# Kernel tuning notes

Hardware: AMD Instinct MI355X
Metric: run time of the kernel (lower is better)

The kernel has to match this reference:

```python
import jax, jax.numpy as jnp
import numpy as np


def setup_inputs() -> dict:
    key = jax.random.key(0)
    kq, kk, kv = jax.random.split(key, 3)
    B, N, D = 16, 2048, 64
    queries = jax.random.normal(kq, (B, N, D), dtype=jnp.float32)
    keys = jax.random.normal(kk, (B, N, D), dtype=jnp.float32)
    values = jax.random.normal(kv, (B, N, D), dtype=jnp.float32)
    return {"queries": queries, "keys": keys, "values": values}


def reference(queries, keys, values):
    d = queries.shape[-1]
    scale = 1.0 / jnp.sqrt(jnp.asarray(d, dtype=queries.dtype))
    # scores: [B, Nq, Nk]
    scores = jnp.einsum("bqd,bkd->bqk", queries, keys) * scale
    # Faithful to the original: softmax over dim=0 (the batch dimension).
    attn = jax.nn.softmax(scores, axis=0)
    # dropout p=0.0 -> identity
    return jnp.einsum("bqk,bkd->bqd", attn, values)
```

## Files before the change

### kernel.cpp

```cpp
#include <hip/hip_runtime.h>
#include <hip/hip_bf16.h>

typedef __attribute__((ext_vector_type(8))) short short8;
typedef __attribute__((ext_vector_type(4))) short short4v;
typedef __attribute__((ext_vector_type(2))) int   int2v;
typedef __attribute__((ext_vector_type(4))) float floatx4;

#define BATCH 16
#define SEQ   2048
#define DIM   64
#define QSCALE 0.18033688011112042f
#define WS_NEED (12u*1024u*1024u)

__device__ __forceinline__ unsigned short f2bf(float f) {
    return __builtin_bit_cast(unsigned short, __float2bfloat16(f));
}

#if defined(__has_builtin)
#if __has_builtin(__builtin_amdgcn_exp2f)
#define EXP2(x) __builtin_amdgcn_exp2f(x)
#endif
#endif
#ifndef EXP2
#define EXP2(x) exp2f(x)
#endif

#define MFMA32(A,B,C) __builtin_amdgcn_mfma_f32_16x16x32_bf16(A,B,C,0,0,0)

#if defined(__has_builtin)
#if __has_builtin(__builtin_amdgcn_mfma_f32_16x16x16bf16_1k)
#define MFMA16(A,B,C) __builtin_amdgcn_mfma_f32_16x16x16bf16_1k(A,B,C,0,0,0)
#elif __has_builtin(__builtin_amdgcn_mfma_f32_16x16x16_bf16)
#define MFMA16(A,B,C) __builtin_amdgcn_mfma_f32_16x16x16_bf16(A,B,C,0,0,0)
#endif
#endif
#ifndef MFMA16
__device__ __forceinline__ floatx4 mfma16_asm(short4v a, short4v b, floatx4 c) {
    asm volatile("s_nop 1\n\tv_mfma_f32_16x16x16_bf16 %0, %1, %2, %0"
                 : "+v"(c) : "v"(a), "v"(b));
    return c;
}
#define MFMA16(A,B,C) mfma16_asm(A,B,C)
#endif

#define LIGHT_BARRIER()                                        \
    do {                                                       \
        asm volatile("s_waitcnt lgkmcnt(0)" ::: "memory");     \
        __builtin_amdgcn_s_barrier();                          \
        __builtin_amdgcn_sched_barrier(0);                     \
    } while (0)

__global__ __launch_bounds__(256)
void convert_kernel(const float* __restrict__ Q, const float* __restrict__ K,
                    const float* __restrict__ V, unsigned short* __restrict__ ws) {
    const int t = blockIdx.x * 256 + threadIdx.x;
    if (t < 524288) {
        const int region = t >> 18;
        const int r = t & 262143;
        const int b = r >> 14;
        const int rem = r & 16383;
        const int t16 = rem >> 7;
        const int st  = (rem >> 6) & 1;
        const int l   = rem & 63;
        const int a = l & 15, g = l >> 4;
        const float* src = (region == 0 ? Q : K) +
            ((size_t)(b * SEQ + t16 * 16 + a)) * DIM + st * 32 + g * 8;
        const float s = (region == 0) ? QSCALE : 1.0f;
        short8 o;
        #pragma unroll
        for (int p = 0; p < 8; ++p) o[p] = (short)f2bf(src[p] * s);
        *(short8*)(ws + (size_t)region * 2097152 + (size_t)r * 8) = o;
    } else {
        const int r = t - 524288;
        const int b  = r >> 13;
        const int kt = (r >> 6) & 127;
        const int l  = r & 63;
        const int a = l & 15, g = l >> 4;
        const float* src = V + ((size_t)(b * SEQ + kt * 16 + g * 4)) * DIM + a;
        short8 o0, o1;
        #pragma unroll
        for (int dt = 0; dt < 2; ++dt)
            #pragma unroll
            for (int p = 0; p < 4; ++p)
                o0[dt * 4 + p] = (short)f2bf(src[(size_t)p * DIM + dt * 16]);
        #pragma unroll
        for (int dt = 2; dt < 4; ++dt)
            #pragma unroll
            for (int p = 0; p < 4; ++p)
                o1[(dt - 2) * 4 + p] = (short)f2bf(src[(size_t)p * DIM + dt * 16]);
        unsigned short* dst = ws + 4194304 + (size_t)r * 16;
        *(short8*)(dst)     = o0;
        *(short8*)(dst + 8) = o1;
    }
}

__global__ __launch_bounds__(512)
void dpa_main(const unsigned short* __restrict__ Qw, const unsigned short* __restrict__ Kw,
              const unsigned short* __restrict__ Vw, float* __restrict__ Og) {
    __shared__ __align__(16) float dl[2][4][64][12];

    const int tid = threadIdx.x;
    const int l = tid & 63;
    const int w = tid >> 6;
    const int a = l & 15, g = l >> 4;
    const int bx = blockIdx.x;
    const int ch = bx & 3;
    const int qt = bx >> 2;
    const int b0 = w * 2;
    const int wsw = w ^ (l >> 3);

    const unsigned short* Kb = Kw + (size_t)b0 * 131072 + l * 8;
    const unsigned short* Vb = Vw + (size_t)b0 * 131072 + l * 16;

    short8 Qf[2][2];
    {
        const unsigned short* Qb = Qw + (size_t)b0 * 131072 + qt * 1024 + l * 8;
        #pragma unroll
        for (int bb = 0; bb < 2; ++bb)
            #pragma unroll
            for (int st = 0; st < 2; ++st)
                Qf[bb][st] = *(const short8*)(Qb + bb * 131072 + st * 512);
    }

    short8 Kf[2][2];
    #pragma unroll
    for (int bb = 0; bb < 2; ++bb)
        #pragma unroll
        for (int st = 0; st < 2; ++st)
            Kf[bb][st] = *(const short8*)(Kb + bb * 131072 + (ch * 32) * 1024 + st * 512);

    floatx4 O[2][4];
    #pragma unroll
    for (int bb = 0; bb < 2; ++bb)
        #pragma unroll
        for (int dt = 0; dt < 4; ++dt) O[bb][dt] = (floatx4)0.0f;

    floatx4 SA[2], SB[2];

#define QKEXP(T, SOUT)                                                        \
    __builtin_amdgcn_s_setprio(1);                                            \
    {                                                                         \
        floatx4 s0 = (floatx4)0.0f, s1 = (floatx4)0.0f;                       \
        s0 = MFMA32(Kf[0][0], Qf[0][0], s0);                                  \
        s0 = MFMA32(Kf[0][1], Qf[0][1], s0);                                  \
        s1 = MFMA32(Kf[1][0], Qf[1][0], s1);                                  \
        s1 = MFMA32(Kf[1][1], Qf[1][1], s1);                                  \
        SOUT[0] = s0; SOUT[1] = s1;                                           \
    }                                                                         \
    __builtin_amdgcn_s_setprio(0);                                            \
    {                                                                         \
        const int ktn_ = ch * 32 + (((T) < 31) ? (T) + 1 : 31);               \
        Kf[0][0] = *(const short8*)(Kb + 0 * 131072 + ktn_ * 1024);           \
        Kf[0][1] = *(const short8*)(Kb + 0 * 131072 + ktn_ * 1024 + 512);     \
        Kf[1][0] = *(const short8*)(Kb + 1 * 131072 + ktn_ * 1024);           \
        Kf[1][1] = *(const short8*)(Kb + 1 * 131072 + ktn_ * 1024 + 512);     \
    }                                                                         \
    _Pragma("unroll")                                                         \
    for (int r = 0; r < 4; ++r) {                                             \
        const float e0 = EXP2(SOUT[0][r]);                                    \
        const float e1 = EXP2(SOUT[1][r]);                                    \
        SOUT[0][r] = e0; SOUT[1][r] = e1;                                     \
        dl[(T) & 1][r][l][wsw] = e0 + e1;                                     \
    }

#define COMBINE_PV(T, SPREV, v01_0, v23_0, v01_1, v23_1)                      \
    {                                                                         \
        float fr_[4];                                                         \
        _Pragma("unroll")                                                     \
        for (int r = 0; r < 4; ++r) {                                         \
            const floatx4 u0 = *(const floatx4*)&dl[((T)-1) & 1][r][l][0];    \
            const floatx4 u1 = *(const floatx4*)&dl[((T)-1) & 1][r][l][4];    \
            const floatx4 us = u0 + u1;                                       \
            fr_[r] = __builtin_amdgcn_rcpf((us[0] + us[1]) + (us[2] + us[3]));\
        }                                                                     \
        _Pragma("unroll")                                                     \
        for (int bb = 0; bb < 2; ++bb) {                                      \
            const short8 v01 = (bb == 0) ? v01_0 : v01_1;                     \
            const short8 v23 = (bb == 0) ? v23_0 : v23_1;                     \
            const unsigned int c0 = __builtin_bit_cast(unsigned int, SPREV[bb][0] * fr_[0]) + 0x8000u; \
            const unsigned int c1 = __builtin_bit_cast(unsigned int, SPREV[bb][1] * fr_[1]) + 0x8000u; \
            const unsigned int c2 = __builtin_bit_cast(unsigned int, SPREV[bb][2] * fr_[2]) + 0x8000u; \
            const unsigned int c3 = __builtin_bit_cast(unsigned int, SPREV[bb][3] * fr_[3]) + 0x8000u; \
            int2v pp;                                                         \
            pp[0] = (int)__builtin_amdgcn_perm(c1, c0, 0x07060302u);          \
            pp[1] = (int)__builtin_amdgcn_perm(c3, c2, 0x07060302u);          \
            const short4v af = __builtin_bit_cast(short4v, pp);               \
            const short4v b0v = __builtin_shufflevector(v01, v01, 0, 1, 2, 3);\
            const short4v b1v = __builtin_shufflevector(v01, v01, 4, 5, 6, 7);\
            const short4v b2v = __builtin_shufflevector(v23, v23, 0, 1, 2, 3);\
            const short4v b3v = __builtin_shufflevector(v23, v23, 4, 5, 6, 7);\
            __builtin_amdgcn_s_setprio(1);                                    \
            O[bb][0] = MFMA16(af, b0v, O[bb][0]);                             \
            O[bb][1] = MFMA16(af, b1v, O[bb][1]);                             \
            O[bb][2] = MFMA16(af, b2v, O[bb][2]);                             \
            O[bb][3] = MFMA16(af, b3v, O[bb][3]);                             \
            __builtin_amdgcn_s_setprio(0);                                    \
        }                                                                     \
    }

#define BODY(T, SOUT, SPREV)                                                  \
    {                                                                         \
        const int ktp_ = ch * 32 + (T) - 1;                                   \
        const unsigned short* vp0_ = Vb + 0 * 131072 + ktp_ * 1024;           \
        const unsigned short* vp1_ = Vb + 1 * 131072 + ktp_ * 1024;           \
        const short8 V01_0_ = *(const short8*)(vp0_);                         \
        const short8 V23_0_ = *(const short8*)(vp0_ + 8);                     \
        const short8 V01_1_ = *(const short8*)(vp1_);                         \
        const short8 V23_1_ = *(const short8*)(vp1_ + 8);                     \
        QKEXP(T, SOUT)                                                        \
        LIGHT_BARRIER();                                                      \
        COMBINE_PV(T, SPREV, V01_0_, V23_0_, V01_1_, V23_1_)                  \
        LIGHT_BARRIER();                                                      \
    }

    QKEXP(0, SA)

    #pragma unroll 1
    for (int j = 0; j < 15; ++j) {
        const int t1 = 2 * j + 1;
        BODY(t1, SB, SA)
        BODY(t1 + 1, SA, SB)
    }
    BODY(31, SB, SA)

    {
        const int ktp = ch * 32 + 31;
        const unsigned short* vp0 = Vb + 0 * 131072 + ktp * 1024;
        const unsigned short* vp1 = Vb + 1 * 131072 + ktp * 1024;
        const short8 V01_0 = *(const short8*)(vp0);
        const short8 V23_0 = *(const short8*)(vp0 + 8);
        const short8 V01_1 = *(const short8*)(vp1);
        const short8 V23_1 = *(const short8*)(vp1 + 8);
        COMBINE_PV(32, SB, V01_0, V23_0, V01_1, V23_1)
    }

    asm volatile("s_nop 7\n\ts_nop 7" :::);

    #pragma unroll
    for (int bb = 0; bb < 2; ++bb)
        #pragma unroll
        for (int dt = 0; dt < 4; ++dt)
            #pragma unroll
            for (int r = 0; r < 4; ++r)
                unsafeAtomicAdd(Og + ((size_t)((b0 + bb) * SEQ + qt * 16 + g * 4 + r)) * DIM
                                    + dt * 16 + a,
                                O[bb][dt][r]);
#undef BODY
#undef COMBINE_PV
#undef QKEXP
}

__global__ __launch_bounds__(512)
void dpa_naive(const float* __restrict__ Q, const float* __restrict__ K,
               const float* __restrict__ V, float* __restrict__ out) {
    __shared__ float attn_lds[BATCH][8][64];
    const int tid = threadIdx.x;
    const int lane_k = tid & 63, row_q = tid >> 6, lane_d = tid & 63;
    const int q0 = blockIdx.x * 8;
    float acc[BATCH];
    #pragma unroll
    for (int b = 0; b < BATCH; ++b) acc[b] = 0.0f;
    for (int k0 = 0; k0 < SEQ; k0 += 64) {
        float s[BATCH];
        #pragma unroll
        for (int b = 0; b < BATCH; ++b) {
            const float4* qrow = (const float4*)(Q + ((size_t)b * SEQ + (q0 + row_q)) * DIM);
            const float4* krow = (const float4*)(K + ((size_t)b * SEQ + (k0 + lane_k)) * DIM);
            float a0 = 0.f;
            #pragma unroll
            for (int d4 = 0; d4 < 16; ++d4) {
                float4 qa = qrow[d4]; float4 kb = krow[d4];
                a0 += qa.x*kb.x + qa.y*kb.y + qa.z*kb.z + qa.w*kb.w;
            }
            s[b] = a0 * 0.125f;
        }
        float m = s[0];
        #pragma unroll
        for (int b = 1; b < BATCH; ++b) m = fmaxf(m, s[b]);
        float den = 0.f;
        #pragma unroll
        for (int b = 0; b < BATCH; ++b) { s[b] = __expf(s[b] - m); den += s[b]; }
        const float inv = 1.0f / den;
        #pragma unroll
        for (int b = 0; b < BATCH; ++b) attn_lds[b][row_q][lane_k] = s[b] * inv;
        __syncthreads();
        #pragma unroll
        for (int b = 0; b < BATCH; ++b) {
            const float* vbase = V + ((size_t)b * SEQ + k0) * DIM + lane_d;
            float acc2 = 0.f;
            #pragma unroll 8
            for (int kk = 0; kk < 64; ++kk) acc2 += attn_lds[b][row_q][kk] * vbase[(size_t)kk * DIM];
            acc[b] += acc2;
        }
        __syncthreads();
    }
    #pragma unroll
    for (int b = 0; b < BATCH; ++b)
        out[((size_t)b * SEQ + (q0 + row_q)) * DIM + lane_d] = acc[b];
}

extern "C" void kernel_launch(void* const* d_in, const int* in_sizes, int n_in,
                              void* d_out, int out_size, void* d_ws, size_t ws_size,
                              hipStream_t stream) {
    const float* Q = (const float*)d_in[0];
    const float* K = (const float*)d_in[1];
    const float* V = (const float*)d_in[2];
    float* out = (float*)d_out;

    if (ws_size < WS_NEED) {
        dpa_naive<<<dim3(SEQ / 8), dim3(512), 0, stream>>>(Q, K, V, out);
        return;
    }
    unsigned short* ws = (unsigned short*)d_ws;
    hipMemsetAsync(d_out, 0, (size_t)out_size * sizeof(float), stream);
    convert_kernel<<<dim3(2560), dim3(256), 0, stream>>>(Q, K, V, ws);
    dpa_main<<<dim3(512), dim3(512), 0, stream>>>(ws, ws + 2097152, ws + 4194304, out);
}
```

Measured before the change: 82.59 us.

## Process two key tiles per barrier phase to halve workgroup barriers

Restructures the main loop so each iteration computes QK and exp for two key tiles, then does one barrier and two combine/PV steps, with a double-buffered LDS partial-sum array indexed by iteration parity. The software pipeline across single tiles is replaced by a two-tile batch, with two K register sets prefetched. The goal is to cut the number of LIGHT_BARRIER syncs per tile in half, at the cost of more registers, a larger LDS buffer, and less overlap between QK of the next tile and PV of the current one.

```diff
diff --git a/kernel.cpp b/kernel.cpp
--- a/kernel.cpp
+++ b/kernel.cpp
@@ -97,7 +97,7 @@
 __global__ __launch_bounds__(512)
 void dpa_main(const unsigned short* __restrict__ Qw, const unsigned short* __restrict__ Kw,
               const unsigned short* __restrict__ Vw, float* __restrict__ Og) {
-    __shared__ __align__(16) float dl[2][4][64][12];
+    __shared__ __align__(16) float dl[2][8][64][12];
 
     const int tid = threadIdx.x;
     const int l = tid & 63;
@@ -122,12 +122,14 @@
                 Qf[bb][st] = *(const short8*)(Qb + bb * 131072 + st * 512);
     }
 
-    short8 Kf[2][2];
+    short8 Kf0[2][2], Kf1[2][2];
     #pragma unroll
     for (int bb = 0; bb < 2; ++bb)
         #pragma unroll
-        for (int st = 0; st < 2; ++st)
-            Kf[bb][st] = *(const short8*)(Kb + bb * 131072 + (ch * 32) * 1024 + st * 512);
+        for (int st = 0; st < 2; ++st) {
+            Kf0[bb][st] = *(const short8*)(Kb + bb * 131072 + (ch * 32 + 0) * 1024 + st * 512);
+            Kf1[bb][st] = *(const short8*)(Kb + bb * 131072 + (ch * 32 + 1) * 1024 + st * 512);
+        }
 
     floatx4 O[2][4];
     #pragma unroll
@@ -135,41 +137,35 @@
         #pragma unroll
         for (int dt = 0; dt < 4; ++dt) O[bb][dt] = (floatx4)0.0f;
 
-    floatx4 SA[2], SB[2];
-
-#define QKEXP(T, SOUT)                                                        \
-    __builtin_amdgcn_s_setprio(1);                                            \
+#define QKTILE(KF, SOUT, KTN, SLOT, P)                                        \
     {                                                                         \
         floatx4 s0 = (floatx4)0.0f, s1 = (floatx4)0.0f;                       \
-        s0 = MFMA32(Kf[0][0], Qf[0][0], s0);                                  \
-        s0 = MFMA32(Kf[0][1], Qf[0][1], s0);                                  \
-        s1 = MFMA32(Kf[1][0], Qf[1][0], s1);                                  \
-        s1 = MFMA32(Kf[1][1], Qf[1][1], s1);                                  \
-        SOUT[0] = s0; SOUT[1] = s1;                                           \
-    }                                                                         \
-    __builtin_amdgcn_s_setprio(0);                                            \
-    {                                                                         \
-        const int ktn_ = ch * 32 + (((T) < 31) ? (T) + 1 : 31);               \
-        Kf[0][0] = *(const short8*)(Kb + 0 * 131072 + ktn_ * 1024);           \
-        Kf[0][1] = *(const short8*)(Kb + 0 * 131072 + ktn_ * 1024 + 512);     \
-        Kf[1][0] = *(const short8*)(Kb + 1 * 131072 + ktn_ * 1024);           \
-        Kf[1][1] = *(const short8*)(Kb + 1 * 131072 + ktn_ * 1024 + 512);     \
-    }                                                                         \
-    _Pragma("unroll")                                                         \
-    for (int r = 0; r < 4; ++r) {                                             \
-        const float e0 = EXP2(SOUT[0][r]);                                    \
-        const float e1 = EXP2(SOUT[1][r]);                                    \
-        SOUT[0][r] = e0; SOUT[1][r] = e1;                                     \
-        dl[(T) & 1][r][l][wsw] = e0 + e1;                                     \
-    }
-
-#define COMBINE_PV(T, SPREV, v01_0, v23_0, v01_1, v23_1)                      \
+        __builtin_amdgcn_s_setprio(1);                                        \
+        s0 = MFMA32(KF[0][0], Qf[0][0], s0);                                  \
+        s0 = MFMA32(KF[0][1], Qf[0][1], s0);                                  \
+        s1 = MFMA32(KF[1][0], Qf[1][0], s1);                                  \
+        s1 = MFMA32(KF[1][1], Qf[1][1], s1);                                  \
+        __builtin_amdgcn_s_setprio(0);                                        \
+        KF[0][0] = *(const short8*)(Kb + 0 * 131072 + (KTN) * 1024);          \
+        KF[0][1] = *(const short8*)(Kb + 0 * 131072 + (KTN) * 1024 + 512);    \
+        KF[1][0] = *(const short8*)(Kb + 1 * 131072 + (KTN) * 1024);          \
+        KF[1][1] = *(const short8*)(Kb + 1 * 131072 + (KTN) * 1024 + 512);    \
+        _Pragma("unroll")                                                     \
+        for (int r = 0; r < 4; ++r) {                                         \
+            const float e0 = EXP2(s0[r]);                                     \
+            const float e1 = EXP2(s1[r]);                                     \
+            SOUT[0][r] = e0; SOUT[1][r] = e1;                                 \
+            dl[P][(SLOT) + r][l][wsw] = e0 + e1;                              \
+        }                                                                     \
+    }
+
+#define COMBINE_PV(SPREV, SLOT, P, v01_0, v23_0, v01_1, v23_1)                \
     {                                                                         \
         float fr_[4];                                                         \
         _Pragma("unroll")                                                     \
         for (int r = 0; r < 4; ++r) {                                         \
-            const floatx4 u0 = *(const floatx4*)&dl[((T)-1) & 1][r][l][0];    \
-            const floatx4 u1 = *(const floatx4*)&dl[((T)-1) & 1][r][l][4];    \
+            const floatx4 u0 = *(const floatx4*)&dl[P][(SLOT) + r][l][0];     \
+            const floatx4 u1 = *(const floatx4*)&dl[P][(SLOT) + r][l][4];     \
             const floatx4 us = u0 + u1;                                       \
             fr_[r] = __builtin_amdgcn_rcpf((us[0] + us[1]) + (us[2] + us[3]));\
         }                                                                     \
@@ -198,40 +194,39 @@
         }                                                                     \
     }
 
-#define BODY(T, SOUT, SPREV)                                                  \
-    {                                                                         \
-        const int ktp_ = ch * 32 + (T) - 1;                                   \
-        const unsigned short* vp0_ = Vb + 0 * 131072 + ktp_ * 1024;           \
-        const unsigned short* vp1_ = Vb + 1 * 131072 + ktp_ * 1024;           \
-        const short8 V01_0_ = *(const short8*)(vp0_);                         \
-        const short8 V23_0_ = *(const short8*)(vp0_ + 8);                     \
-        const short8 V01_1_ = *(const short8*)(vp1_);                         \
-        const short8 V23_1_ = *(const short8*)(vp1_ + 8);                     \
-        QKEXP(T, SOUT)                                                        \
-        LIGHT_BARRIER();                                                      \
-        COMBINE_PV(T, SPREV, V01_0_, V23_0_, V01_1_, V23_1_)                  \
-        LIGHT_BARRIER();                                                      \
-    }
-
-    QKEXP(0, SA)
+    floatx4 S0[2], S1[2];
 
     #pragma unroll 1
-    for (int j = 0; j < 15; ++j) {
-        const int t1 = 2 * j + 1;
-        BODY(t1, SB, SA)
-        BODY(t1 + 1, SA, SB)
-    }
-    BODY(31, SB, SA)
-
-    {
-        const int ktp = ch * 32 + 31;
-        const unsigned short* vp0 = Vb + 0 * 131072 + ktp * 1024;
-        const unsigned short* vp1 = Vb + 1 * 131072 + ktp * 1024;
-        const short8 V01_0 = *(const short8*)(vp0);
-        const short8 V23_0 = *(const short8*)(vp0 + 8);
-        const short8 V01_1 = *(const short8*)(vp1);
-        const short8 V23_1 = *(const short8*)(vp1 + 8);
-        COMBINE_PV(32, SB, V01_0, V23_0, V01_1, V23_1)
+    for (int j = 0; j < 16; ++j) {
+        const int p = j & 1;
+        const int kt0 = ch * 32 + 2 * j;
+        const int kt1 = kt0 + 1;
+        const int ktn0 = (j < 15) ? (kt0 + 2) : kt0;
+        const int ktn1 = (j < 15) ? (kt1 + 2) : kt1;
+
+        short8 V01_0[2], V23_0[2];
+        #pragma unroll
+        for (int bb = 0; bb < 2; ++bb) {
+            const unsigned short* vp = Vb + bb * 131072 + kt0 * 1024;
+            V01_0[bb] = *(const short8*)(vp);
+            V23_0[bb] = *(const short8*)(vp + 8);
+        }
+
+        QKTILE(Kf0, S0, ktn0, 0, p)
+        QKTILE(Kf1, S1, ktn1, 4, p)
+        LIGHT_BARRIER();
+
+        COMBINE_PV(S0, 0, p, V01_0[0], V23_0[0], V01_0[1], V23_0[1])
+
+        short8 V01_1[2], V23_1[2];
+        #pragma unroll
+        for (int bb = 0; bb < 2; ++bb) {
+            const unsigned short* vp = Vb + bb * 131072 + kt1 * 1024;
+            V01_1[bb] = *(const short8*)(vp);
+            V23_1[bb] = *(const short8*)(vp + 8);
+        }
+
+        COMBINE_PV(S1, 4, p, V01_1[0], V23_1[0], V01_1[1], V23_1[1])
     }
 
     asm volatile("s_nop 7\n\ts_nop 7" :::);
@@ -245,9 +240,8 @@
                 unsafeAtomicAdd(Og + ((size_t)((b0 + bb) * SEQ + qt * 16 + g * 4 + r)) * DIM
                                     + dt * 16 + a,
                                 O[bb][dt][r]);
-#undef BODY
 #undef COMBINE_PV
-#undef QKEXP
+#undef QKTILE
 }
 
 __global__ __launch_bounds__(512)
```

New measurement: 87.17 us. +5.5%, slower.

## Fold Q conversion into main kernel and output zeroing into KV convert

Applied to the files above, without the earlier changes.

Q is no longer pre-converted to bf16 in a separate pass. Each wave in the main kernel loads its fp32 Q fragment directly, scales it and converts it in registers. The output memset is folded into the K/V conversion kernel, which drops one launch and shrinks the workspace. The cost is that each Q tile is read as fp32 by the main kernel, a small one-time load per block.

```diff
diff --git a/kernel.cpp b/kernel.cpp
--- a/kernel.cpp
+++ b/kernel.cpp
@@ -10,7 +10,7 @@
 #define SEQ   2048
 #define DIM   64
 #define QSCALE 0.18033688011112042f
-#define WS_NEED (12u*1024u*1024u)
+#define WS_NEED (9u*1024u*1024u)
 
 __device__ __forceinline__ unsigned short f2bf(float f) {
     return __builtin_bit_cast(unsigned short, __float2bfloat16(f));
@@ -51,27 +51,28 @@
     } while (0)
 
 __global__ __launch_bounds__(256)
-void convert_kernel(const float* __restrict__ Q, const float* __restrict__ K,
-                    const float* __restrict__ V, unsigned short* __restrict__ ws) {
+void convert_kv(const float* __restrict__ K, const float* __restrict__ V,
+                unsigned short* __restrict__ ws, float* __restrict__ Og) {
     const int t = blockIdx.x * 256 + threadIdx.x;
-    if (t < 524288) {
-        const int region = t >> 18;
-        const int r = t & 262143;
+
+    for (unsigned u = (unsigned)t; u < 524288u; u += 393216u)
+        ((floatx4*)Og)[u] = (floatx4)0.0f;
+
+    if (t < 262144) {
+        const int r = t;
         const int b = r >> 14;
         const int rem = r & 16383;
         const int t16 = rem >> 7;
         const int st  = (rem >> 6) & 1;
         const int l   = rem & 63;
         const int a = l & 15, g = l >> 4;
-        const float* src = (region == 0 ? Q : K) +
-            ((size_t)(b * SEQ + t16 * 16 + a)) * DIM + st * 32 + g * 8;
-        const float s = (region == 0) ? QSCALE : 1.0f;
+        const float* src = K + ((size_t)(b * SEQ + t16 * 16 + a)) * DIM + st * 32 + g * 8;
         short8 o;
         #pragma unroll
-        for (int p = 0; p < 8; ++p) o[p] = (short)f2bf(src[p] * s);
-        *(short8*)(ws + (size_t)region * 2097152 + (size_t)r * 8) = o;
+        for (int p = 0; p < 8; ++p) o[p] = (short)f2bf(src[p]);
+        *(short8*)(ws + (size_t)r * 8) = o;
     } else {
-        const int r = t - 524288;
+        const int r = t - 262144;
         const int b  = r >> 13;
         const int kt = (r >> 6) & 127;
         const int l  = r & 63;
@@ -88,14 +89,14 @@
             #pragma unroll
             for (int p = 0; p < 4; ++p)
                 o1[(dt - 2) * 4 + p] = (short)f2bf(src[(size_t)p * DIM + dt * 16]);
-        unsigned short* dst = ws + 4194304 + (size_t)r * 16;
+        unsigned short* dst = ws + 2097152 + (size_t)r * 16;
         *(short8*)(dst)     = o0;
         *(short8*)(dst + 8) = o1;
     }
 }
 
 __global__ __launch_bounds__(512)
-void dpa_main(const unsigned short* __restrict__ Qw, const unsigned short* __restrict__ Kw,
+void dpa_main(const float* __restrict__ Qg, const unsigned short* __restrict__ Kw,
               const unsigned short* __restrict__ Vw, float* __restrict__ Og) {
     __shared__ __align__(16) float dl[2][4][64][12];
 
@@ -113,13 +114,21 @@
     const unsigned short* Vb = Vw + (size_t)b0 * 131072 + l * 16;
 
     short8 Qf[2][2];
-    {
-        const unsigned short* Qb = Qw + (size_t)b0 * 131072 + qt * 1024 + l * 8;
-        #pragma unroll
-        for (int bb = 0; bb < 2; ++bb)
-            #pragma unroll
-            for (int st = 0; st < 2; ++st)
-                Qf[bb][st] = *(const short8*)(Qb + bb * 131072 + st * 512);
+    #pragma unroll
+    for (int bb = 0; bb < 2; ++bb) {
+        #pragma unroll
+        for (int st = 0; st < 2; ++st) {
+            const float* src = Qg + ((size_t)((b0 + bb) * SEQ + qt * 16 + a)) * DIM
+                                  + st * 32 + g * 8;
+            const float4 f0 = *(const float4*)(src);
+            const float4 f1 = *(const float4*)(src + 4);
+            short8 q;
+            q[0] = (short)f2bf(f0.x * QSCALE); q[1] = (short)f2bf(f0.y * QSCALE);
+            q[2] = (short)f2bf(f0.z * QSCALE); q[3] = (short)f2bf(f0.w * QSCALE);
+            q[4] = (short)f2bf(f1.x * QSCALE); q[5] = (short)f2bf(f1.y * QSCALE);
+            q[6] = (short)f2bf(f1.z * QSCALE); q[7] = (short)f2bf(f1.w * QSCALE);
+            Qf[bb][st] = q;
+        }
     }
 
     short8 Kf[2][2];
@@ -312,7 +321,6 @@
         return;
     }
     unsigned short* ws = (unsigned short*)d_ws;
-    hipMemsetAsync(d_out, 0, (size_t)out_size * sizeof(float), stream);
-    convert_kernel<<<dim3(2560), dim3(256), 0, stream>>>(Q, K, V, ws);
-    dpa_main<<<dim3(512), dim3(512), 0, stream>>>(ws, ws + 2097152, ws + 4194304, out);
-}
+    convert_kv<<<dim3(1536), dim3(256), 0, stream>>>(K, V, ws, out);
+    dpa_main<<<dim3(512), dim3(512), 0, stream>>>(Q, ws, ws + 2097152, out);
+}
```

New measurement: 96.15 us. 1.16x slower.
